# Performance work log

Measured on AMD Instinct MI355X. Metric: run time of the kernel, lower is better.

The kernel has to match this reference:

```python
import jax, jax.numpy as jnp
import numpy as np

# SLAYER neuron/simulation constants (netParams)
THETA = 10.0      # spike threshold
TAU_SR = 10.0     # PSP (SRM alpha) time constant
TAU_REF = 1.0     # refractory time constant
TAU_RHO = 1.0     # surrogate-gradient width
SCALE_RHO = 1.0   # surrogate-gradient scale
TS = 1.0          # simulation timestep
K_EPS = 100       # truncated FIR length of the alpha PSP kernel
REF_DECAY = float(np.exp(-TS / TAU_REF))


@jax.custom_vjp
def _spike_fn(v):
    # heaviside threshold with SLAYER-style exponential surrogate gradient
    return (v >= 0.0).astype(v.dtype)

def _spike_fwd(v):
    return (v >= 0.0).astype(v.dtype), v

def _spike_bwd(v, g):
    return (g * (SCALE_RHO / TAU_RHO) * jnp.exp(-jnp.abs(v) / TAU_RHO),)

_spike_fn.defvjp(_spike_fwd, _spike_bwd)


def psp(x):
    """Causal temporal filter with SRM alpha kernel eps(t)=(t/tau)exp(1-t/tau)."""
    shp = x.shape
    T = shp[-1]
    t = jnp.arange(K_EPS, dtype=x.dtype) * TS
    eps = (t / TAU_SR) * jnp.exp(1.0 - t / TAU_SR)
    xr = x.reshape(-1, 1, T)  # [N,1,T]
    y = jax.lax.conv_general_dilated(xr, eps[::-1].reshape(1, 1, K_EPS), (1,), [(K_EPS - 1, 0)])
    return y.reshape(shp)


def spike(u):
    """Sequential threshold with decaying refractory state (scan over time)."""
    uT = jnp.moveaxis(u, -1, 0)  # [T, ...]

    def step(r, u_t):
        s = _spike_fn(u_t + r - THETA)
        return REF_DECAY * r - 2.0 * THETA * s, s

    _, sT = jax.lax.scan(step, jnp.zeros(uT.shape[1:], uT.dtype), uT)
    return jnp.moveaxis(sT, 0, -1)


def pool(x, k):
    # SLAYER pool: fixed-weight sum conv, weight = 1.1*theta/(k*k) per element
    B, C, H, W, T = x.shape
    return x.reshape(B, C, H // k, k, W // k, k, T).sum(axis=(3, 5)) * (1.1 * THETA / (k * k))


def conv(x, w, pad):
    # 3D conv with time-pointwise kernel == per-timestep 2D conv (fold T into batch)
    B, C, H, W, T = x.shape
    xr = jnp.moveaxis(x, -1, 1).reshape(B * T, C, H, W)
    y = jax.lax.conv_general_dilated(xr, w, (1, 1), [(pad, pad), (pad, pad)])
    return jnp.moveaxis(y.reshape(B, T, w.shape[0], H, W), 1, -1)


def delay(x, d):
    """Per-channel learnable temporal delay via linear interpolation gather."""
    T = x.shape[-1]
    C = d.shape[0]
    t = jnp.arange(T, dtype=x.dtype)
    src = t[None, :] - d[:, None]            # [C, T]
    i0 = jnp.floor(src)
    w = (src - i0).reshape((1, C, 1, 1, T))
    i0 = i0.astype(jnp.int32)

    def take(idx):
        v = jnp.take_along_axis(x, jnp.clip(idx, 0, T - 1).reshape((1, C, 1, 1, T)), axis=-1)
        ok = ((idx >= 0) & (idx < T)).reshape((1, C, 1, 1, T))
        return jnp.where(ok, v, 0.0)

    return take(i0) * (1.0 - w) + take(i0 + 1) * w


def setup_inputs() -> dict:
    key = jax.random.key(0)
    ks = jax.random.split(key, 9)
    B, T = 4, 300
    spikeInput = (jax.random.uniform(ks[0], (B, 2, 128, 128, T)) < 0.03).astype(jnp.float32)
    conv1_w = jax.random.normal(ks[1], (16, 2, 5, 5), jnp.float32) * (1.0 / np.sqrt(2 * 25))
    conv2_w = jax.random.normal(ks[2], (32, 16, 3, 3), jnp.float32) * (1.0 / np.sqrt(16 * 9))
    fc1_w = jax.random.normal(ks[3], (512, 2048), jnp.float32) * (1.0 / np.sqrt(2048))
    fc2_w = jax.random.normal(ks[4], (11, 512), jnp.float32) * (1.0 / np.sqrt(512))
    delay1_d = jax.random.uniform(ks[5], (16,), jnp.float32) * 4.0
    delay2_d = jax.random.uniform(ks[6], (32,), jnp.float32) * 4.0
    delay3_d = jax.random.uniform(ks[7], (512,), jnp.float32) * 4.0
    return {"spikeInput": spikeInput, "conv1_w": conv1_w, "conv2_w": conv2_w,
            "fc1_w": fc1_w, "fc2_w": fc2_w,
            "delay1_d": delay1_d, "delay2_d": delay2_d, "delay3_d": delay3_d}


def reference(spikeInput, conv1_w, conv2_w, fc1_w, fc2_w, delay1_d, delay2_d, delay3_d):
    s = spike(pool(psp(spikeInput), 4))          # [B,2,32,32,T]
    s = spike(conv(psp(s), conv1_w, 2))          # [B,16,32,32,T]
    s = delay(s, delay1_d)
    s = spike(pool(psp(s), 2))                   # [B,16,16,16,T]
    s = spike(conv(psp(s), conv2_w, 1))          # [B,32,16,16,T]
    s = delay(s, delay2_d)
    s = spike(pool(psp(s), 2))                   # [B,32,8,8,T]
    B, C, H, W, T = s.shape
    s = s.reshape(B, C * H * W, 1, 1, T)         # [B,2048,1,1,T]
    s = spike(jnp.einsum('oi,bixyt->boxyt', fc1_w, psp(s)))  # [B,512,1,1,T]
    s = delay(s, delay3_d)
    s = spike(jnp.einsum('oi,bixyt->boxyt', fc2_w, psp(s)))  # [B,11,1,1,T]
    return s
```

## Files before the change

### kernel.cpp

```cpp
#include <hip/hip_runtime.h>

#define TLEN 300
#define THETA 10.0f
#define REF_DECAY 0.36787944117144233f

#define QS 101
#define WS 404
#define DQ 25

__global__ void eps_init_kernel(float* __restrict__ eps) {
  int k = threadIdx.x;
  if (k < 104) eps[k] = 0.f;
  if (k < 100) {
    float a = (float)k / 10.0f;
    eps[k] = a * expf(1.0f - a);
  }
}

#define FIRSTEP(e, A, B, C)                                                              \
  acc[0] += e.x * B.x; acc[1] += e.x * B.y; acc[2] += e.x * B.z; acc[3] += e.x * B.w;    \
  acc[4] += e.x * C.x; acc[5] += e.x * C.y; acc[6] += e.x * C.z; acc[7] += e.x * C.w;    \
  acc[0] += e.y * A.w; acc[1] += e.y * B.x; acc[2] += e.y * B.y; acc[3] += e.y * B.z;    \
  acc[4] += e.y * B.w; acc[5] += e.y * C.x; acc[6] += e.y * C.y; acc[7] += e.y * C.z;    \
  acc[0] += e.z * A.z; acc[1] += e.z * A.w; acc[2] += e.z * B.x; acc[3] += e.z * B.y;    \
  acc[4] += e.z * B.z; acc[5] += e.z * B.w; acc[6] += e.z * C.x; acc[7] += e.z * C.y;    \
  acc[0] += e.w * A.y; acc[1] += e.w * A.z; acc[2] += e.w * A.w; acc[3] += e.w * B.x;    \
  acc[4] += e.w * B.y; acc[5] += e.w * B.z; acc[6] += e.w * B.w; acc[7] += e.w * C.x;

__device__ __forceinline__ void fir100s(const float4* __restrict__ row4, int l,
                                        const float* __restrict__ epss, float acc[8]) {
  const int qB = DQ + 2 * l;
  float4 A = row4[qB - 1];
  float4 B = row4[qB];
  float4 C = row4[qB + 1];
#pragma unroll
  for (int j = 0; j < 8; ++j) acc[j] = 0.f;
#pragma unroll 1
  for (int kg0 = 0; kg0 < 80; kg0 += 20) {
    const float* ep = epss + kg0;
    const float4* ap = row4 + (qB - 2 - (kg0 >> 2));
#pragma unroll
    for (int kk = 0; kk < 5; ++kk) {
      const float4 e = *reinterpret_cast<const float4*>(ep + 4 * kk);
      FIRSTEP(e, A, B, C);
      C = B; B = A;
      A = ap[-kk];
    }
    __builtin_amdgcn_sched_barrier(0);
  }
#pragma unroll
  for (int kk = 0; kk < 5; ++kk) {
    const float4 e = *reinterpret_cast<const float4*>(epss + 80 + 4 * kk);
    FIRSTEP(e, A, B, C);
    C = B; B = A;
    if (kk < 4) A = row4[qB - 22 - kk];
  }
}

__device__ __forceinline__ void psp_init_pads(float4* xs, float4* xs2, float* epss,
                                              const float* __restrict__ epsg, int tid) {
  if (tid < 104) epss[tid] = epsg[tid];
  if (tid < 208) {
    int r = tid / 26, k = tid - r * 26;
    int q = (k < 25) ? k : 100;
    xs[r * QS + q] = make_float4(0.f, 0.f, 0.f, 0.f);
    xs2[r * QS + q] = make_float4(0.f, 0.f, 0.f, 0.f);
  }
}

__device__ __forceinline__ void fir1_lds(const float4* xs, float4* xs2,
                                         const float* epss, int tid) {
  if (tid < 304) {
    int r = tid & 7, l = tid >> 3;
    float acc[8];
    fir100s(xs + r * QS, l, epss, acc);
    xs2[r * QS + DQ + 2 * l] = make_float4(acc[0], acc[1], acc[2], acc[3]);
    if (l < 37)
      xs2[r * QS + DQ + 2 * l + 1] = make_float4(acc[4], acc[5], acc[6], acc[7]);
  }
}

__device__ __forceinline__ void fir2_out(const float4* xs2, const float* epss,
                                         int tid, float* __restrict__ out, long row0) {
  if (tid < 304) {
    int r = tid & 7, l = tid >> 3;
    float acc[8];
    fir100s(xs2 + r * QS, l, epss, acc);
    long off = (row0 + r) * TLEN + 8 * l;
    *reinterpret_cast<float4*>(out + off) = make_float4(acc[0], acc[1], acc[2], acc[3]);
    if (l < 37)
      *reinterpret_cast<float4*>(out + off + 4) = make_float4(acc[4], acc[5], acc[6], acc[7]);
  }
}

__device__ __forceinline__ void scan8(float4* buf, int tid) {
  if (tid < 8) {
    float ref = 0.f;
    float4* row = buf + tid * QS + DQ;
#pragma unroll 1
    for (int c4 = 0; c4 < 75; ++c4) {
      float4 u = row[c4];
      float v, sp;
      v = u.x + ref - THETA; sp = (v >= 0.f) ? 1.f : 0.f; u.x = sp; ref = REF_DECAY * ref - 20.0f * sp;
      v = u.y + ref - THETA; sp = (v >= 0.f) ? 1.f : 0.f; u.y = sp; ref = REF_DECAY * ref - 20.0f * sp;
      v = u.z + ref - THETA; sp = (v >= 0.f) ? 1.f : 0.f; u.z = sp; ref = REF_DECAY * ref - 20.0f * sp;
      v = u.w + ref - THETA; sp = (v >= 0.f) ? 1.f : 0.f; u.w = sp; ref = REF_DECAY * ref - 20.0f * sp;
      row[c4] = u;
    }
  }
}

__global__ __launch_bounds__(320, 4) void psp_spike_psp_kernel(const float* __restrict__ in,
                                                               float* __restrict__ out,
                                                               const float* __restrict__ epsg) {
  __shared__ float4 xs[8 * QS];
  __shared__ float4 xs2[8 * QS];
  __shared__ float epss[104];
  const int tid = threadIdx.x;
  const long row0 = (long)blockIdx.x * 8;
  psp_init_pads(xs, xs2, epss, epsg, tid);
  for (int i = tid; i < 600; i += 320) {
    int r = i / 75, q = i - r * 75;
    xs[r * QS + DQ + q] =
        *reinterpret_cast<const float4*>(in + (row0 + r) * TLEN + 4 * q);
  }
  __syncthreads();
  fir1_lds(xs, xs2, epss, tid);
  __syncthreads();
  scan8(xs2, tid);
  __syncthreads();
  fir2_out(xs2, epss, tid, out, row0);
}

__global__ __launch_bounds__(320, 4) void pool4_psp_spike_psp_kernel(
    const float* __restrict__ in, float* __restrict__ out, const float* __restrict__ epsg) {
  __shared__ float4 xs[8 * QS];
  __shared__ float4 xs2[8 * QS];
  __shared__ float epss[104];
  const int tid = threadIdx.x;
  const long row0 = (long)blockIdx.x * 8;
  psp_init_pads(xs, xs2, epss, epsg, tid);
  for (int i = tid; i < 600; i += 320) {
    int r = i / 75, q = i - r * 75;
    long orow = row0 + r;
    int bc = (int)(orow >> 10);
    int y = (int)((orow >> 5) & 31);
    int x = (int)(orow & 31);
    const float* base = in + ((long)(bc * 128 + y * 4) * 128 + x * 4) * TLEN + 4 * q;
    float4 s = make_float4(0.f, 0.f, 0.f, 0.f);
#pragma unroll
    for (int dy = 0; dy < 4; ++dy)
#pragma unroll
      for (int dx = 0; dx < 4; ++dx) {
        float4 v = *reinterpret_cast<const float4*>(base + (dy * 128 + dx) * TLEN);
        s.x += v.x; s.y += v.y; s.z += v.z; s.w += v.w;
      }
    s.x *= 0.6875f; s.y *= 0.6875f; s.z *= 0.6875f; s.w *= 0.6875f;
    xs[r * QS + DQ + q] = s;
  }
  __syncthreads();
  fir1_lds(xs, xs2, epss, tid);
  __syncthreads();
  scan8(xs2, tid);
  __syncthreads();
  fir2_out(xs2, epss, tid, out, row0);
}

__global__ __launch_bounds__(320, 4) void reduce_spike_delay_psp_kernel(
    const float* __restrict__ part, const float* __restrict__ dly,
    float* __restrict__ out, const float* __restrict__ epsg) {
  __shared__ float4 xs[8 * QS];
  __shared__ float4 xs2[8 * QS];
  __shared__ float epss[104];
  const int tid = threadIdx.x;
  const long row0 = (long)blockIdx.x * 8;
  psp_init_pads(xs, xs2, epss, epsg, tid);
  for (int i = tid; i < 600; i += 320) {
    int r = i / 75, q = i - r * 75;
    long off = (row0 + r) * TLEN + 4 * q;
    const float4 v0 = *reinterpret_cast<const float4*>(part + off);
    const float4 v1 = *reinterpret_cast<const float4*>(part + 614400 + off);
    const float4 v2 = *reinterpret_cast<const float4*>(part + 1228800 + off);
    const float4 v3 = *reinterpret_cast<const float4*>(part + 1843200 + off);
    float4 v;
    v.x = (v0.x + v1.x) + (v2.x + v3.x);
    v.y = (v0.y + v1.y) + (v2.y + v3.y);
    v.z = (v0.z + v1.z) + (v2.z + v3.z);
    v.w = (v0.w + v1.w) + (v2.w + v3.w);
    xs[r * QS + DQ + q] = v;
  }
  __syncthreads();
  scan8(xs, tid);
  __syncthreads();
  const float* xf = reinterpret_cast<const float*>(xs);
  for (int i = tid; i < 600; i += 320) {
    int r = i / 75, q = i - r * 75;
    float dd = dly[(int)((row0 + r) & 511)];
    float4 o;
    float* op = &o.x;
#pragma unroll
    for (int j = 0; j < 4; ++j) {
      int t = 4 * q + j;
      float src = (float)t - dd;
      float fi = floorf(src);
      int i0 = (int)fi;
      float wf = src - fi;
      float v0 = xf[r * WS + 100 + i0];
      float v1 = xf[r * WS + 101 + i0];
      op[j] = v0 * (1.f - wf) + v1 * wf;
    }
    xs2[r * QS + DQ + q] = o;
  }
  __syncthreads();
  fir2_out(xs2, epss, tid, out, row0);
}

__device__ __forceinline__ int sqz(int r, int q) { return (q & ~7) | ((q + r) & 7); }

__global__ __launch_bounds__(256) void spike_pool2_delay_kernel(const float* __restrict__ u,
                                                                const float* __restrict__ dly,
                                                                float* __restrict__ out,
                                                                int WI, int C) {
  __shared__ float4 ch[64 * 16];
  __shared__ unsigned int bits[64 * 13];
  const int tid = threadIdx.x;
  const long inrow0 = (long)blockIdx.x * 64;
  float ref = 0.f;
  unsigned int wbits = 0;
  for (int cix = 0; cix < 5; ++cix) {
    __syncthreads();
    for (int i = tid; i < 960; i += 256) {
      int r = i / 15, q = i - r * 15;
      ch[r * 16 + sqz(r, q)] = *reinterpret_cast<const float4*>(
          u + (inrow0 + r) * TLEN + cix * 60 + 4 * q);
    }
    __syncthreads();
    if (tid < 64) {
      int r = tid;
#pragma unroll 1
      for (int q = 0; q < 15; ++q) {
        float4 v = ch[r * 16 + sqz(r, q)];
        int t = cix * 60 + 4 * q;
        float x, sp;
        x = v.x + ref - THETA; sp = (x >= 0.f) ? 1.f : 0.f; ref = REF_DECAY * ref - 20.0f * sp;
        wbits |= ((unsigned int)sp) << (t & 31);
        if ((t & 31) == 31) { bits[r * 13 + (t >> 5)] = wbits; wbits = 0; }
        x = v.y + ref - THETA; sp = (x >= 0.f) ? 1.f : 0.f; ref = REF_DECAY * ref - 20.0f * sp;
        wbits |= ((unsigned int)sp) << ((t + 1) & 31);
        if (((t + 1) & 31) == 31) { bits[r * 13 + ((t + 1) >> 5)] = wbits; wbits = 0; }
        x = v.z + ref - THETA; sp = (x >= 0.f) ? 1.f : 0.f; ref = REF_DECAY * ref - 20.0f * sp;
        wbits |= ((unsigned int)sp) << ((t + 2) & 31);
        if (((t + 2) & 31) == 31) { bits[r * 13 + ((t + 2) >> 5)] = wbits; wbits = 0; }
        x = v.w + ref - THETA; sp = (x >= 0.f) ? 1.f : 0.f; ref = REF_DECAY * ref - 20.0f * sp;
        wbits |= ((unsigned int)sp) << ((t + 3) & 31);
        if (((t + 3) & 31) == 31) { bits[r * 13 + ((t + 3) >> 5)] = wbits; wbits = 0; }
      }
    }
  }
  if (tid < 64) bits[tid * 13 + 9] = wbits;
  __syncthreads();
  const int WO = WI >> 1;
  const int bc = (int)(inrow0 / (WI * WI));
  const int y0 = (int)((inrow0 % (WI * WI)) / WI);
  const float dd = dly[bc % C];
  const long orow0 = (long)bc * (WO * WO) + (y0 >> 1) * WO;
  for (int i = tid; i < 4800; i += 256) {
    int ro = i / TLEN, t = i - ro * TLEN;
    int Yr = ro / WO, X = ro - Yr * WO;
    int ir = (2 * Yr) * WI + 2 * X;
    float src = (float)t - dd;
    float fi = floorf(src);
    int i0 = (int)fi;
    float wf = src - fi;
    bool ok0 = (i0 >= 0) && (i0 < TLEN);
    bool ok1 = (i0 + 1 >= 0) && (i0 + 1 < TLEN);
    int j0 = min(max(i0, 0), TLEN - 1);
    int j1 = min(max(i0 + 1, 0), TLEN - 1);
    int s0i = 0, s1i = 0;
#pragma unroll
    for (int dy = 0; dy < 2; ++dy)
#pragma unroll
      for (int dx = 0; dx < 2; ++dx) {
        int rr = ir + dy * WI + dx;
        s0i += (int)((bits[rr * 13 + (j0 >> 5)] >> (j0 & 31)) & 1u);
        s1i += (int)((bits[rr * 13 + (j1 >> 5)] >> (j1 & 31)) & 1u);
      }
    float s0 = ok0 ? (float)s0i : 0.f;
    float s1 = ok1 ? (float)s1i : 0.f;
    out[(orow0 + ro) * TLEN + t] = (s0 * (1.f - wf) + s1 * wf) * 2.75f;
  }
}

__global__ __launch_bounds__(256) void conv1_kernel(const float* __restrict__ in,
                                                    const float* __restrict__ w,
                                                    float* __restrict__ out) {
  __shared__ float xl[11520];
  const int tid = threadIdx.x;
  const int t0 = blockIdx.x * 32;
  const int y = blockIdx.y;
  const int b = blockIdx.z;
  for (int i = tid; i < 2880; i += 256) {
    int tq = i & 7;
    int rest = i >> 3;
    int xp = rest % 36;
    int r2 = rest / 36;
    int dy = r2 % 5;
    int c = r2 / 5;
    int yy = y + dy - 2, xx = xp - 2, t = t0 + tq * 4;
    float4 v = {0.f, 0.f, 0.f, 0.f};
    if (yy >= 0 && yy < 32 && xx >= 0 && xx < 32 && t < TLEN)
      v = *reinterpret_cast<const float4*>(
          in + ((long)((b * 2 + c) * 32 + yy) * 32 + xx) * TLEN + t);
    *reinterpret_cast<float4*>(&xl[rest * 32 + tq * 4]) = v;
  }
  __syncthreads();
  const int tg = tid & 7;
  const int x = tid >> 3;
  float acc[16][4];
#pragma unroll
  for (int o = 0; o < 16; ++o) { acc[o][0] = acc[o][1] = acc[o][2] = acc[o][3] = 0.f; }
  for (int c = 0; c < 2; ++c)
#pragma unroll
    for (int dy = 0; dy < 5; ++dy)
#pragma unroll
      for (int kx = 0; kx < 5; ++kx) {
        const float4 xv = *reinterpret_cast<const float4*>(
            &xl[((c * 5 + dy) * 36 + x + kx) * 32 + tg * 4]);
        const float* wp = w + (c * 5 + dy) * 5 + kx;
#pragma unroll
        for (int o = 0; o < 16; ++o) {
          float wsc = wp[o * 50];
          acc[o][0] += wsc * xv.x; acc[o][1] += wsc * xv.y;
          acc[o][2] += wsc * xv.z; acc[o][3] += wsc * xv.w;
        }
      }
  const int t = t0 + tg * 4;
  if (t < TLEN) {
#pragma unroll
    for (int o = 0; o < 16; ++o) {
      float4 res; res.x = acc[o][0]; res.y = acc[o][1]; res.z = acc[o][2]; res.w = acc[o][3];
      *reinterpret_cast<float4*>(&out[((long)((b * 16 + o) * 32 + y) * 32 + x) * TLEN + t]) = res;
    }
  }
}

__global__ __launch_bounds__(256) void conv2_kernel(const float* __restrict__ in,
                                                    const float* __restrict__ w,
                                                    float* __restrict__ out) {
  __shared__ float xl[13824];
  const int tid = threadIdx.x;
  const int t0 = blockIdx.x * 16;
  const int y = blockIdx.y;
  const int b = blockIdx.z;
  for (int i = tid; i < 3456; i += 256) {
    int tq = i & 3;
    int rest = i >> 2;
    int xp = rest % 18;
    int r2 = rest / 18;
    int dy = r2 % 3;
    int c = r2 / 3;
    int yy = y + dy - 1, xx = xp - 1, t = t0 + tq * 4;
    float4 v = {0.f, 0.f, 0.f, 0.f};
    if (yy >= 0 && yy < 16 && xx >= 0 && xx < 16 && t < TLEN)
      v = *reinterpret_cast<const float4*>(
          in + ((long)((b * 16 + c) * 16 + yy) * 16 + xx) * TLEN + t);
    *reinterpret_cast<float4*>(&xl[rest * 16 + tq * 4]) = v;
  }
  __syncthreads();
  const int tg = tid & 3;
  const int x = (tid >> 2) & 15;
  const int oh = tid >> 6;
  float acc[8][4];
#pragma unroll
  for (int o = 0; o < 8; ++o) { acc[o][0] = acc[o][1] = acc[o][2] = acc[o][3] = 0.f; }
  for (int c = 0; c < 16; ++c)
#pragma unroll
    for (int dy = 0; dy < 3; ++dy)
#pragma unroll
      for (int kx = 0; kx < 3; ++kx) {
        const float4 xv = *reinterpret_cast<const float4*>(
            &xl[((c * 3 + dy) * 18 + x + kx) * 16 + tg * 4]);
        const float* wp = w + (c * 3 + dy) * 3 + kx;
#pragma unroll
        for (int oo = 0; oo < 8; ++oo) {
          float wsc = wp[(oh * 8 + oo) * 144];
          acc[oo][0] += wsc * xv.x; acc[oo][1] += wsc * xv.y;
          acc[oo][2] += wsc * xv.z; acc[oo][3] += wsc * xv.w;
        }
      }
  const int t = t0 + tg * 4;
  if (t < TLEN) {
#pragma unroll
    for (int oo = 0; oo < 8; ++oo) {
      int o = oh * 8 + oo;
      float4 res; res.x = acc[oo][0]; res.y = acc[oo][1]; res.z = acc[oo][2]; res.w = acc[oo][3];
      *reinterpret_cast<float4*>(&out[((long)((b * 32 + o) * 16 + y) * 16 + x) * TLEN + t]) = res;
    }
  }
}

__global__ __launch_bounds__(256) void fc1_kernel(const float* __restrict__ x,
                                                  const float* __restrict__ w,
                                                  float* __restrict__ part) {
  __shared__ float wl[64][44];
  __shared__ float xlb[32][68];
  const int tid = threadIdx.x;
  const int t0 = blockIdx.x * 64;
  const int o0 = blockIdx.y * 64;
  const int b = blockIdx.z >> 2;
  const int split = blockIdx.z & 3;
  const int tx = tid & 15, ty = tid >> 4;
  float acc[4][4];
#pragma unroll
  for (int i = 0; i < 4; ++i)
#pragma unroll
    for (int j = 0; j < 4; ++j) acc[i][j] = 0.f;
  const int kbeg = split * 512;
  for (int kc = kbeg; kc < kbeg + 512; kc += 32) {
    __syncthreads();
#pragma unroll
    for (int rr = 0; rr < 2; ++rr) {
      int i = rr * 256 + tid;
      int ol = i >> 3, kq = i & 7;
      float4 v = *reinterpret_cast<const float4*>(w + (long)(o0 + ol) * 2048 + kc + kq * 4);
      *reinterpret_cast<float4*>(&wl[ol][kq * 4]) = v;
    }
#pragma unroll
    for (int rr = 0; rr < 2; ++rr) {
      int i = rr * 256 + tid;
      int kl = i >> 4, tq = i & 15;
      int t = t0 + tq * 4;
      float4 v = {0.f, 0.f, 0.f, 0.f};
      if (t < TLEN)
        v = *reinterpret_cast<const float4*>(x + ((long)b * 2048 + kc + kl) * TLEN + t);
      *reinterpret_cast<float4*>(&xlb[kl][tq * 4]) = v;
    }
    __syncthreads();
#pragma unroll
    for (int k4 = 0; k4 < 8; ++k4) {
      float4 wq[4], xq[4];
#pragma unroll
      for (int i = 0; i < 4; ++i)
        wq[i] = *reinterpret_cast<const float4*>(&wl[ty * 4 + i][k4 * 4]);
#pragma unroll
      for (int j = 0; j < 4; ++j)
        xq[j] = *reinterpret_cast<const float4*>(&xlb[k4 * 4 + j][tx * 4]);
#pragma unroll
      for (int i = 0; i < 4; ++i) {
        float wa[4] = {wq[i].x, wq[i].y, wq[i].z, wq[i].w};
#pragma unroll
        for (int j = 0; j < 4; ++j) {
          float xa[4] = {xq[j].x, xq[j].y, xq[j].z, xq[j].w};
          acc[i][0] += wa[j] * xa[0]; acc[i][1] += wa[j] * xa[1];
          acc[i][2] += wa[j] * xa[2]; acc[i][3] += wa[j] * xa[3];
        }
      }
    }
  }
  const int t = t0 + tx * 4;
  if (t < TLEN) {
#pragma unroll
    for (int i = 0; i < 4; ++i) {
      float4 res; res.x = acc[i][0]; res.y = acc[i][1]; res.z = acc[i][2]; res.w = acc[i][3];
      *reinterpret_cast<float4*>(
          part + ((long)(split * 4 + b) * 512 + o0 + ty * 4 + i) * TLEN + t) = res;
    }
  }
}

__global__ __launch_bounds__(320) void fc2_spike_kernel(const float* __restrict__ x,
                                                        const float* __restrict__ w,
                                                        float* __restrict__ out) {
  __shared__ float ul[304];
  int blk = blockIdx.x;
  int b = blk / 11, o = blk % 11;
  int t = threadIdx.x;
  if (t < TLEN) {
    const float* xr = x + (long)b * 512 * TLEN + t;
    const float* wr = w + o * 512;
    float a0 = 0.f, a1 = 0.f, a2 = 0.f, a3 = 0.f;
#pragma unroll 4
    for (int i = 0; i < 512; i += 4) {
      a0 += wr[i] * xr[(long)i * TLEN];
      a1 += wr[i + 1] * xr[(long)(i + 1) * TLEN];
      a2 += wr[i + 2] * xr[(long)(i + 2) * TLEN];
      a3 += wr[i + 3] * xr[(long)(i + 3) * TLEN];
    }
    ul[t] = (a0 + a1) + (a2 + a3);
  }
  __syncthreads();
  if (t == 0) {
    float ref = 0.f;
#pragma unroll 4
    for (int c = 0; c < TLEN; ++c) {
      float v = ul[c] + ref - THETA;
      float sp = (v >= 0.f) ? 1.f : 0.f;
      ul[c] = sp;
      ref = REF_DECAY * ref - 20.0f * sp;
    }
  }
  __syncthreads();
  if (t < TLEN) out[((long)b * 11 + o) * TLEN + t] = ul[t];
}

extern "C" void kernel_launch(void* const* d_in, const int* in_sizes, int n_in,
                              void* d_out, int out_size, void* d_ws, size_t ws_size,
                              hipStream_t stream) {
  const float* input = (const float*)d_in[0];
  const float* w1    = (const float*)d_in[1];
  const float* w2    = (const float*)d_in[2];
  const float* wfc1  = (const float*)d_in[3];
  const float* wfc2  = (const float*)d_in[4];
  const float* d1    = (const float*)d_in[5];
  const float* d2    = (const float*)d_in[6];
  const float* d3    = (const float*)d_in[7];

  float* ws   = (float*)d_ws;
  float* big0 = ws;
  float* medA = big0 + 19660800;
  float* medB = medA + 4915200;
  float* fcA  = medB + 4915200;
  float* fcB  = fcA + 614400;
  float* eps  = fcB + 614400;

  hipLaunchKernelGGL(eps_init_kernel, dim3(1), dim3(128), 0, stream, eps);

  hipLaunchKernelGGL(pool4_psp_spike_psp_kernel, dim3(1024), dim3(320), 0, stream,
                     input, medB, eps);
  hipLaunchKernelGGL(conv1_kernel, dim3(10, 32, 4), dim3(256), 0, stream, medB, w1, big0);
  hipLaunchKernelGGL(spike_pool2_delay_kernel, dim3(1024), dim3(256), 0, stream,
                     big0, d1, medA, 32, 16);
  hipLaunchKernelGGL(psp_spike_psp_kernel, dim3(2048), dim3(320), 0, stream, medA, medB, eps);
  hipLaunchKernelGGL(conv2_kernel, dim3(19, 16, 4), dim3(256), 0, stream, medB, w2, big0);
  hipLaunchKernelGGL(spike_pool2_delay_kernel, dim3(512), dim3(256), 0, stream,
                     big0, d2, medA, 16, 32);
  hipLaunchKernelGGL(psp_spike_psp_kernel, dim3(1024), dim3(320), 0, stream, medA, medB, eps);
  hipLaunchKernelGGL(fc1_kernel, dim3(5, 8, 16), dim3(256), 0, stream, medB, wfc1, big0);
  hipLaunchKernelGGL(reduce_spike_delay_psp_kernel, dim3(256), dim3(320), 0, stream,
                     big0, d3, fcA, eps);
  hipLaunchKernelGGL(fc2_spike_kernel, dim3(44), dim3(320), 0, stream, fcA, wfc2, (float*)d_out);
}
```

Measured before the change: 481.6 us.

## Split fused psp/spike/pool/delay kernels into separate simple kernels

Replaces the fused pool+psp+spike+psp, spike+pool2+delay and reduce+spike+delay+psp kernels with standalone pool4, fir, scan, pool2_delay, scan_reduce4 and fir_delay kernels. The scan runs per-row in its own kernel reading global memory directly with register prefetch, and the spike bit-packing in LDS is dropped. This simplifies each stage, but it adds kernel launches and global-memory round trips between stages, and the scan kernels launch few threads.

```diff
diff --git a/kernel.cpp b/kernel.cpp
--- a/kernel.cpp
+++ b/kernel.cpp
@@ -5,7 +5,6 @@
 #define REF_DECAY 0.36787944117144233f
 
 #define QS 101
-#define WS 404
 #define DQ 25
 
 __global__ void eps_init_kernel(float* __restrict__ eps) {
@@ -57,35 +56,28 @@
   }
 }
 
-__device__ __forceinline__ void psp_init_pads(float4* xs, float4* xs2, float* epss,
-                                              const float* __restrict__ epsg, int tid) {
+__global__ __launch_bounds__(320, 4) void fir_kernel(const float* __restrict__ in,
+                                                     float* __restrict__ out,
+                                                     const float* __restrict__ epsg) {
+  __shared__ float4 xs[8 * QS];
+  __shared__ float epss[104];
+  const int tid = threadIdx.x;
+  const long row0 = (long)blockIdx.x * 8;
   if (tid < 104) epss[tid] = epsg[tid];
   if (tid < 208) {
     int r = tid / 26, k = tid - r * 26;
     int q = (k < 25) ? k : 100;
     xs[r * QS + q] = make_float4(0.f, 0.f, 0.f, 0.f);
-    xs2[r * QS + q] = make_float4(0.f, 0.f, 0.f, 0.f);
-  }
-}
-
-__device__ __forceinline__ void fir1_lds(const float4* xs, float4* xs2,
-                                         const float* epss, int tid) {
+  }
+  for (int i = tid; i < 600; i += 320) {
+    int r = i / 75, q = i - r * 75;
+    xs[r * QS + DQ + q] = *reinterpret_cast<const float4*>(in + (row0 + r) * TLEN + 4 * q);
+  }
+  __syncthreads();
   if (tid < 304) {
     int r = tid & 7, l = tid >> 3;
     float acc[8];
     fir100s(xs + r * QS, l, epss, acc);
-    xs2[r * QS + DQ + 2 * l] = make_float4(acc[0], acc[1], acc[2], acc[3]);
-    if (l < 37)
-      xs2[r * QS + DQ + 2 * l + 1] = make_float4(acc[4], acc[5], acc[6], acc[7]);
-  }
-}
-
-__device__ __forceinline__ void fir2_out(const float4* xs2, const float* epss,
-                                         int tid, float* __restrict__ out, long row0) {
-  if (tid < 304) {
-    int r = tid & 7, l = tid >> 3;
-    float acc[8];
-    fir100s(xs2 + r * QS, l, epss, acc);
     long off = (row0 + r) * TLEN + 8 * l;
     *reinterpret_cast<float4*>(out + off) = make_float4(acc[0], acc[1], acc[2], acc[3]);
     if (l < 37)
@@ -93,109 +85,25 @@
   }
 }
 
-__device__ __forceinline__ void scan8(float4* buf, int tid) {
-  if (tid < 8) {
-    float ref = 0.f;
-    float4* row = buf + tid * QS + DQ;
-#pragma unroll 1
-    for (int c4 = 0; c4 < 75; ++c4) {
-      float4 u = row[c4];
-      float v, sp;
-      v = u.x + ref - THETA; sp = (v >= 0.f) ? 1.f : 0.f; u.x = sp; ref = REF_DECAY * ref - 20.0f * sp;
-      v = u.y + ref - THETA; sp = (v >= 0.f) ? 1.f : 0.f; u.y = sp; ref = REF_DECAY * ref - 20.0f * sp;
-      v = u.z + ref - THETA; sp = (v >= 0.f) ? 1.f : 0.f; u.z = sp; ref = REF_DECAY * ref - 20.0f * sp;
-      v = u.w + ref - THETA; sp = (v >= 0.f) ? 1.f : 0.f; u.w = sp; ref = REF_DECAY * ref - 20.0f * sp;
-      row[c4] = u;
-    }
-  }
-}
-
-__global__ __launch_bounds__(320, 4) void psp_spike_psp_kernel(const float* __restrict__ in,
-                                                               float* __restrict__ out,
-                                                               const float* __restrict__ epsg) {
+__global__ __launch_bounds__(320, 4) void fir_delay_kernel(const float* __restrict__ in,
+                                                           float* __restrict__ out,
+                                                           const float* __restrict__ epsg,
+                                                           const float* __restrict__ dly) {
   __shared__ float4 xs[8 * QS];
-  __shared__ float4 xs2[8 * QS];
   __shared__ float epss[104];
   const int tid = threadIdx.x;
   const long row0 = (long)blockIdx.x * 8;
-  psp_init_pads(xs, xs2, epss, epsg, tid);
+  if (tid < 104) epss[tid] = epsg[tid];
+  if (tid < 208) {
+    int r = tid / 26, k = tid - r * 26;
+    int q = (k < 25) ? k : 100;
+    xs[r * QS + q] = make_float4(0.f, 0.f, 0.f, 0.f);
+  }
   for (int i = tid; i < 600; i += 320) {
     int r = i / 75, q = i - r * 75;
-    xs[r * QS + DQ + q] =
-        *reinterpret_cast<const float4*>(in + (row0 + r) * TLEN + 4 * q);
-  }
-  __syncthreads();
-  fir1_lds(xs, xs2, epss, tid);
-  __syncthreads();
-  scan8(xs2, tid);
-  __syncthreads();
-  fir2_out(xs2, epss, tid, out, row0);
-}
-
-__global__ __launch_bounds__(320, 4) void pool4_psp_spike_psp_kernel(
-    const float* __restrict__ in, float* __restrict__ out, const float* __restrict__ epsg) {
-  __shared__ float4 xs[8 * QS];
-  __shared__ float4 xs2[8 * QS];
-  __shared__ float epss[104];
-  const int tid = threadIdx.x;
-  const long row0 = (long)blockIdx.x * 8;
-  psp_init_pads(xs, xs2, epss, epsg, tid);
-  for (int i = tid; i < 600; i += 320) {
-    int r = i / 75, q = i - r * 75;
-    long orow = row0 + r;
-    int bc = (int)(orow >> 10);
-    int y = (int)((orow >> 5) & 31);
-    int x = (int)(orow & 31);
-    const float* base = in + ((long)(bc * 128 + y * 4) * 128 + x * 4) * TLEN + 4 * q;
-    float4 s = make_float4(0.f, 0.f, 0.f, 0.f);
-#pragma unroll
-    for (int dy = 0; dy < 4; ++dy)
-#pragma unroll
-      for (int dx = 0; dx < 4; ++dx) {
-        float4 v = *reinterpret_cast<const float4*>(base + (dy * 128 + dx) * TLEN);
-        s.x += v.x; s.y += v.y; s.z += v.z; s.w += v.w;
-      }
-    s.x *= 0.6875f; s.y *= 0.6875f; s.z *= 0.6875f; s.w *= 0.6875f;
-    xs[r * QS + DQ + q] = s;
-  }
-  __syncthreads();
-  fir1_lds(xs, xs2, epss, tid);
-  __syncthreads();
-  scan8(xs2, tid);
-  __syncthreads();
-  fir2_out(xs2, epss, tid, out, row0);
-}
-
-__global__ __launch_bounds__(320, 4) void reduce_spike_delay_psp_kernel(
-    const float* __restrict__ part, const float* __restrict__ dly,
-    float* __restrict__ out, const float* __restrict__ epsg) {
-  __shared__ float4 xs[8 * QS];
-  __shared__ float4 xs2[8 * QS];
-  __shared__ float epss[104];
-  const int tid = threadIdx.x;
-  const long row0 = (long)blockIdx.x * 8;
-  psp_init_pads(xs, xs2, epss, epsg, tid);
-  for (int i = tid; i < 600; i += 320) {
-    int r = i / 75, q = i - r * 75;
-    long off = (row0 + r) * TLEN + 4 * q;
-    const float4 v0 = *reinterpret_cast<const float4*>(part + off);
-    const float4 v1 = *reinterpret_cast<const float4*>(part + 614400 + off);
-    const float4 v2 = *reinterpret_cast<const float4*>(part + 1228800 + off);
-    const float4 v3 = *reinterpret_cast<const float4*>(part + 1843200 + off);
-    float4 v;
-    v.x = (v0.x + v1.x) + (v2.x + v3.x);
-    v.y = (v0.y + v1.y) + (v2.y + v3.y);
-    v.z = (v0.z + v1.z) + (v2.z + v3.z);
-    v.w = (v0.w + v1.w) + (v2.w + v3.w);
-    xs[r * QS + DQ + q] = v;
-  }
-  __syncthreads();
-  scan8(xs, tid);
-  __syncthreads();
-  const float* xf = reinterpret_cast<const float*>(xs);
-  for (int i = tid; i < 600; i += 320) {
-    int r = i / 75, q = i - r * 75;
-    float dd = dly[(int)((row0 + r) & 511)];
+    long row = row0 + r;
+    float dd = dly[(int)(row & 511)];
+    const float* rowp = in + row * TLEN;
     float4 o;
     float* op = &o.x;
 #pragma unroll
@@ -205,90 +113,127 @@
       float fi = floorf(src);
       int i0 = (int)fi;
       float wf = src - fi;
-      float v0 = xf[r * WS + 100 + i0];
-      float v1 = xf[r * WS + 101 + i0];
+      float v0 = (i0 >= 0 && i0 < TLEN) ? rowp[min(max(i0, 0), TLEN - 1)] : 0.f;
+      float v1 = (i0 + 1 >= 0 && i0 + 1 < TLEN) ? rowp[min(max(i0 + 1, 0), TLEN - 1)] : 0.f;
       op[j] = v0 * (1.f - wf) + v1 * wf;
     }
-    xs2[r * QS + DQ + q] = o;
-  }
-  __syncthreads();
-  fir2_out(xs2, epss, tid, out, row0);
-}
-
-__device__ __forceinline__ int sqz(int r, int q) { return (q & ~7) | ((q + r) & 7); }
-
-__global__ __launch_bounds__(256) void spike_pool2_delay_kernel(const float* __restrict__ u,
-                                                                const float* __restrict__ dly,
-                                                                float* __restrict__ out,
-                                                                int WI, int C) {
-  __shared__ float4 ch[64 * 16];
-  __shared__ unsigned int bits[64 * 13];
-  const int tid = threadIdx.x;
-  const long inrow0 = (long)blockIdx.x * 64;
+    xs[r * QS + DQ + q] = o;
+  }
+  __syncthreads();
+  if (tid < 304) {
+    int r = tid & 7, l = tid >> 3;
+    float acc[8];
+    fir100s(xs + r * QS, l, epss, acc);
+    long off = (row0 + r) * TLEN + 8 * l;
+    *reinterpret_cast<float4*>(out + off) = make_float4(acc[0], acc[1], acc[2], acc[3]);
+    if (l < 37)
+      *reinterpret_cast<float4*>(out + off + 4) = make_float4(acc[4], acc[5], acc[6], acc[7]);
+  }
+}
+
+__global__ __launch_bounds__(64) void scan_kernel(float* __restrict__ u, long rows) {
+  long row = (long)blockIdx.x * 64 + threadIdx.x;
+  if (row >= rows) return;
+  float* p = u + row * TLEN;
+  float4 q0 = *reinterpret_cast<const float4*>(p);
+  float4 q1 = *reinterpret_cast<const float4*>(p + 4);
+  float4 q2 = *reinterpret_cast<const float4*>(p + 8);
+  float4 q3 = *reinterpret_cast<const float4*>(p + 12);
   float ref = 0.f;
-  unsigned int wbits = 0;
-  for (int cix = 0; cix < 5; ++cix) {
-    __syncthreads();
-    for (int i = tid; i < 960; i += 256) {
-      int r = i / 15, q = i - r * 15;
-      ch[r * 16 + sqz(r, q)] = *reinterpret_cast<const float4*>(
-          u + (inrow0 + r) * TLEN + cix * 60 + 4 * q);
-    }
-    __syncthreads();
-    if (tid < 64) {
-      int r = tid;
-#pragma unroll 1
-      for (int q = 0; q < 15; ++q) {
-        float4 v = ch[r * 16 + sqz(r, q)];
-        int t = cix * 60 + 4 * q;
-        float x, sp;
-        x = v.x + ref - THETA; sp = (x >= 0.f) ? 1.f : 0.f; ref = REF_DECAY * ref - 20.0f * sp;
-        wbits |= ((unsigned int)sp) << (t & 31);
-        if ((t & 31) == 31) { bits[r * 13 + (t >> 5)] = wbits; wbits = 0; }
-        x = v.y + ref - THETA; sp = (x >= 0.f) ? 1.f : 0.f; ref = REF_DECAY * ref - 20.0f * sp;
-        wbits |= ((unsigned int)sp) << ((t + 1) & 31);
-        if (((t + 1) & 31) == 31) { bits[r * 13 + ((t + 1) >> 5)] = wbits; wbits = 0; }
-        x = v.z + ref - THETA; sp = (x >= 0.f) ? 1.f : 0.f; ref = REF_DECAY * ref - 20.0f * sp;
-        wbits |= ((unsigned int)sp) << ((t + 2) & 31);
-        if (((t + 2) & 31) == 31) { bits[r * 13 + ((t + 2) >> 5)] = wbits; wbits = 0; }
-        x = v.w + ref - THETA; sp = (x >= 0.f) ? 1.f : 0.f; ref = REF_DECAY * ref - 20.0f * sp;
-        wbits |= ((unsigned int)sp) << ((t + 3) & 31);
-        if (((t + 3) & 31) == 31) { bits[r * 13 + ((t + 3) >> 5)] = wbits; wbits = 0; }
-      }
-    }
-  }
-  if (tid < 64) bits[tid * 13 + 9] = wbits;
-  __syncthreads();
-  const int WO = WI >> 1;
-  const int bc = (int)(inrow0 / (WI * WI));
-  const int y0 = (int)((inrow0 % (WI * WI)) / WI);
-  const float dd = dly[bc % C];
-  const long orow0 = (long)bc * (WO * WO) + (y0 >> 1) * WO;
-  for (int i = tid; i < 4800; i += 256) {
-    int ro = i / TLEN, t = i - ro * TLEN;
-    int Yr = ro / WO, X = ro - Yr * WO;
-    int ir = (2 * Yr) * WI + 2 * X;
-    float src = (float)t - dd;
-    float fi = floorf(src);
-    int i0 = (int)fi;
-    float wf = src - fi;
-    bool ok0 = (i0 >= 0) && (i0 < TLEN);
-    bool ok1 = (i0 + 1 >= 0) && (i0 + 1 < TLEN);
-    int j0 = min(max(i0, 0), TLEN - 1);
-    int j1 = min(max(i0 + 1, 0), TLEN - 1);
-    int s0i = 0, s1i = 0;
-#pragma unroll
-    for (int dy = 0; dy < 2; ++dy)
-#pragma unroll
-      for (int dx = 0; dx < 2; ++dx) {
-        int rr = ir + dy * WI + dx;
-        s0i += (int)((bits[rr * 13 + (j0 >> 5)] >> (j0 & 31)) & 1u);
-        s1i += (int)((bits[rr * 13 + (j1 >> 5)] >> (j1 & 31)) & 1u);
-      }
-    float s0 = ok0 ? (float)s0i : 0.f;
-    float s1 = ok1 ? (float)s1i : 0.f;
-    out[(orow0 + ro) * TLEN + t] = (s0 * (1.f - wf) + s1 * wf) * 2.75f;
-  }
+#pragma unroll 4
+  for (int c4 = 0; c4 < 75; ++c4) {
+    float4 u4 = q0;
+    q0 = q1; q1 = q2; q2 = q3;
+    if (c4 < 71) q3 = *reinterpret_cast<const float4*>(p + 4 * (c4 + 4));
+    float v, sp;
+    v = u4.x + ref - THETA; sp = (v >= 0.f) ? 1.f : 0.f; u4.x = sp; ref = REF_DECAY * ref - 20.0f * sp;
+    v = u4.y + ref - THETA; sp = (v >= 0.f) ? 1.f : 0.f; u4.y = sp; ref = REF_DECAY * ref - 20.0f * sp;
+    v = u4.z + ref - THETA; sp = (v >= 0.f) ? 1.f : 0.f; u4.z = sp; ref = REF_DECAY * ref - 20.0f * sp;
+    v = u4.w + ref - THETA; sp = (v >= 0.f) ? 1.f : 0.f; u4.w = sp; ref = REF_DECAY * ref - 20.0f * sp;
+    *reinterpret_cast<float4*>(p + 4 * c4) = u4;
+  }
+}
+
+__global__ __launch_bounds__(64) void scan_reduce4_kernel(const float* __restrict__ part,
+                                                          float* __restrict__ s) {
+  long row = (long)blockIdx.x * 64 + threadIdx.x;
+  const float* p = part + row * TLEN;
+  float* o = s + row * TLEN;
+  float ref = 0.f;
+#pragma unroll 4
+  for (int c4 = 0; c4 < 75; ++c4) {
+    const float4 v0 = *reinterpret_cast<const float4*>(p + 4 * c4);
+    const float4 v1 = *reinterpret_cast<const float4*>(p + 614400 + 4 * c4);
+    const float4 v2 = *reinterpret_cast<const float4*>(p + 1228800 + 4 * c4);
+    const float4 v3 = *reinterpret_cast<const float4*>(p + 1843200 + 4 * c4);
+    float4 u4;
+    u4.x = (v0.x + v1.x) + (v2.x + v3.x);
+    u4.y = (v0.y + v1.y) + (v2.y + v3.y);
+    u4.z = (v0.z + v1.z) + (v2.z + v3.z);
+    u4.w = (v0.w + v1.w) + (v2.w + v3.w);
+    float v, sp;
+    v = u4.x + ref - THETA; sp = (v >= 0.f) ? 1.f : 0.f; u4.x = sp; ref = REF_DECAY * ref - 20.0f * sp;
+    v = u4.y + ref - THETA; sp = (v >= 0.f) ? 1.f : 0.f; u4.y = sp; ref = REF_DECAY * ref - 20.0f * sp;
+    v = u4.z + ref - THETA; sp = (v >= 0.f) ? 1.f : 0.f; u4.z = sp; ref = REF_DECAY * ref - 20.0f * sp;
+    v = u4.w + ref - THETA; sp = (v >= 0.f) ? 1.f : 0.f; u4.w = sp; ref = REF_DECAY * ref - 20.0f * sp;
+    *reinterpret_cast<float4*>(o + 4 * c4) = u4;
+  }
+}
+
+__global__ __launch_bounds__(256) void pool4_kernel(const float* __restrict__ in,
+                                                    float* __restrict__ out) {
+  int idx = blockIdx.x * 256 + threadIdx.x;
+  if (idx >= 153600) return;
+  int tq = idx % 75;
+  int rest = idx / 75;
+  int x = rest & 31; rest >>= 5;
+  int y = rest & 31; rest >>= 5;
+  const float* base = in + ((long)(rest * 128 + y * 4) * 128 + x * 4) * TLEN + tq * 4;
+  float4 s = {0.f, 0.f, 0.f, 0.f};
+#pragma unroll
+  for (int dy = 0; dy < 4; ++dy)
+#pragma unroll
+    for (int dx = 0; dx < 4; ++dx) {
+      float4 v = *reinterpret_cast<const float4*>(base + (dy * 128 + dx) * TLEN);
+      s.x += v.x; s.y += v.y; s.z += v.z; s.w += v.w;
+    }
+  s.x *= 0.6875f; s.y *= 0.6875f; s.z *= 0.6875f; s.w *= 0.6875f;
+  *reinterpret_cast<float4*>(out + ((long)(rest * 32 + y) * 32 + x) * TLEN + tq * 4) = s;
+}
+
+__global__ __launch_bounds__(256) void pool2_delay_kernel(const float* __restrict__ in,
+                                                          const float* __restrict__ d,
+                                                          float* __restrict__ out,
+                                                          int C, int HO, int WO, int total) {
+  int idx = blockIdx.x * 256 + threadIdx.x;
+  if (idx >= total) return;
+  int t = idx % TLEN;
+  int rest = idx / TLEN;
+  int x = rest % WO; rest /= WO;
+  int y = rest % HO; rest /= HO;
+  int c = rest % C;
+  int b = rest / C;
+  float dd = d[c];
+  float src = (float)t - dd;
+  float fi = floorf(src);
+  int i0 = (int)fi;
+  float wf = src - fi;
+  const float* base = in + (((long)(b * C + c) * (2 * HO) + 2 * y) * (2 * WO) + 2 * x) * TLEN;
+  long rs = (long)(2 * WO) * TLEN;
+  bool ok0 = (i0 >= 0) && (i0 < TLEN);
+  bool ok1 = (i0 + 1 >= 0) && (i0 + 1 < TLEN);
+  int j0 = min(max(i0, 0), TLEN - 1);
+  int j1 = min(max(i0 + 1, 0), TLEN - 1);
+  float s0 = 0.f, s1 = 0.f;
+#pragma unroll
+  for (int dy = 0; dy < 2; ++dy)
+#pragma unroll
+    for (int dx = 0; dx < 2; ++dx) {
+      const float* pp = base + dy * rs + dx * TLEN;
+      s0 += ok0 ? pp[j0] : 0.f;
+      s1 += ok1 ? pp[j1] : 0.f;
+    }
+  out[idx] = (s0 * (1.f - wf) + s1 * wf) * 2.75f;
 }
 
 __global__ __launch_bounds__(256) void conv1_kernel(const float* __restrict__ in,
@@ -525,18 +470,26 @@
 
   hipLaunchKernelGGL(eps_init_kernel, dim3(1), dim3(128), 0, stream, eps);
 
-  hipLaunchKernelGGL(pool4_psp_spike_psp_kernel, dim3(1024), dim3(320), 0, stream,
-                     input, medB, eps);
-  hipLaunchKernelGGL(conv1_kernel, dim3(10, 32, 4), dim3(256), 0, stream, medB, w1, big0);
-  hipLaunchKernelGGL(spike_pool2_delay_kernel, dim3(1024), dim3(256), 0, stream,
-                     big0, d1, medA, 32, 16);
-  hipLaunchKernelGGL(psp_spike_psp_kernel, dim3(2048), dim3(320), 0, stream, medA, medB, eps);
+  hipLaunchKernelGGL(pool4_kernel, dim3(600), dim3(256), 0, stream, input, medA);
+  hipLaunchKernelGGL(fir_kernel, dim3(1024), dim3(320), 0, stream, medA, medB, eps);
+  hipLaunchKernelGGL(scan_kernel, dim3(128), dim3(64), 0, stream, medB, 8192L);
+  hipLaunchKernelGGL(fir_kernel, dim3(1024), dim3(320), 0, stream, medB, medA, eps);
+  hipLaunchKernelGGL(conv1_kernel, dim3(10, 32, 4), dim3(256), 0, stream, medA, w1, big0);
+  hipLaunchKernelGGL(scan_kernel, dim3(1024), dim3(64), 0, stream, big0, 65536L);
+  hipLaunchKernelGGL(pool2_delay_kernel, dim3(19200), dim3(256), 0, stream,
+                     big0, d1, medB, 16, 16, 16, 4915200);
+  hipLaunchKernelGGL(fir_kernel, dim3(2048), dim3(320), 0, stream, medB, medA, eps);
+  hipLaunchKernelGGL(scan_kernel, dim3(256), dim3(64), 0, stream, medA, 16384L);
+  hipLaunchKernelGGL(fir_kernel, dim3(2048), dim3(320), 0, stream, medA, medB, eps);
   hipLaunchKernelGGL(conv2_kernel, dim3(19, 16, 4), dim3(256), 0, stream, medB, w2, big0);
-  hipLaunchKernelGGL(spike_pool2_delay_kernel, dim3(512), dim3(256), 0, stream,
-                     big0, d2, medA, 16, 32);
-  hipLaunchKernelGGL(psp_spike_psp_kernel, dim3(1024), dim3(320), 0, stream, medA, medB, eps);
-  hipLaunchKernelGGL(fc1_kernel, dim3(5, 8, 16), dim3(256), 0, stream, medB, wfc1, big0);
-  hipLaunchKernelGGL(reduce_spike_delay_psp_kernel, dim3(256), dim3(320), 0, stream,
-                     big0, d3, fcA, eps);
-  hipLaunchKernelGGL(fc2_spike_kernel, dim3(44), dim3(320), 0, stream, fcA, wfc2, (float*)d_out);
-}
+  hipLaunchKernelGGL(scan_kernel, dim3(512), dim3(64), 0, stream, big0, 32768L);
+  hipLaunchKernelGGL(pool2_delay_kernel, dim3(9600), dim3(256), 0, stream,
+                     big0, d2, medA, 32, 8, 8, 2457600);
+  hipLaunchKernelGGL(fir_kernel, dim3(1024), dim3(320), 0, stream, medA, medB, eps);
+  hipLaunchKernelGGL(scan_kernel, dim3(128), dim3(64), 0, stream, medB, 8192L);
+  hipLaunchKernelGGL(fir_kernel, dim3(1024), dim3(320), 0, stream, medB, medA, eps);
+  hipLaunchKernelGGL(fc1_kernel, dim3(5, 8, 16), dim3(256), 0, stream, medA, wfc1, big0);
+  hipLaunchKernelGGL(scan_reduce4_kernel, dim3(32), dim3(64), 0, stream, big0, fcA);
+  hipLaunchKernelGGL(fir_delay_kernel, dim3(256), dim3(320), 0, stream, fcA, fcB, eps, d3);
+  hipLaunchKernelGGL(fc2_spike_kernel, dim3(44), dim3(320), 0, stream, fcB, wfc2, (float*)d_out);
+}
```

Result: slower. 545.4 us (+13.2%).
